# Kernel tuning notes

Hardware: AMD Instinct MI355X
Metric: run time of the kernel (lower is better)

## Reference

```python
import jax, jax.numpy as jnp
import numpy as np

B, S, N, E = 8, 32, 512, 8192
RC = DC = 64; SC = 256; EC = 512; P = 12


def setup_inputs() -> dict:
    key = jax.random.key(0)
    ks = jax.random.split(key, 20)
    def rn(k, shape, s=0.05):
        return jax.random.normal(k, shape, jnp.float32) * s
    return {
        "x": jax.random.normal(ks[0], (B, S, N), jnp.float32),
        "edge_index": jax.random.randint(ks[1], (2, E), 0, N),
        "edge_weight": jax.random.uniform(ks[2], (E,), jnp.float32),
        "start_w": rn(ks[3], (RC, 1)), "start_b": rn(ks[4], (RC,)),
        "filt_w": rn(ks[5], (DC, RC, 2)), "filt_b": rn(ks[6], (DC,)),
        "gate_w": rn(ks[7], (DC, RC, 2)), "gate_b": rn(ks[8], (DC,)),
        "gcn_w": rn(ks[9], (DC, DC)), "gcn_b": rn(ks[10], (DC,)),
        "res_w": rn(ks[11], (RC, DC)), "res_b": rn(ks[12], (RC,)),
        "skip_w": rn(ks[13], (SC, DC)), "skip_b": rn(ks[14], (SC,)),
        "end1_w": rn(ks[15], (EC, SC)), "end1_b": rn(ks[16], (EC,)),
        "end2_w": rn(ks[17], (P, EC)), "end2_b": rn(ks[18], (P,)),
    }


def _conv1x1(x, w, b):
    # Conv2d kernel (1,1): pure channel mix. x: [B,C,N,T], w: [O,C]
    return jnp.einsum('bcnt,oc->bont', x, w) + b[None, :, None, None]


def _conv_time2(x, w, b):
    return (jnp.einsum('bcnt,oc->bont', x[..., :-1], w[..., 0])
            + jnp.einsum('bcnt,oc->bont', x[..., 1:], w[..., 1])
            + b[None, :, None, None])


def _gcn_adj(edge_index, edge_weight, n):
    # PyG gcn_norm: add self-loops (weight 1), symmetric D^-1/2 (A+I) D^-1/2,
    # aggregation at edge_index[1] (target). Returns dense A_hat[tgt, src].
    ar = jnp.arange(n)
    row = jnp.concatenate([edge_index[0], ar])
    col = jnp.concatenate([edge_index[1], ar])
    w = jnp.concatenate([edge_weight, jnp.ones((n,), edge_weight.dtype)])
    deg = jnp.zeros((n,), w.dtype).at[col].add(w)
    dis = jnp.where(deg > 0, jax.lax.rsqrt(deg), jnp.zeros_like(deg))
    norm = dis[row] * w * dis[col]
    return jnp.zeros((n, n), w.dtype).at[col, row].add(norm)


def reference(x, edge_index, edge_weight, start_w, start_b, filt_w, filt_b,
              gate_w, gate_b, gcn_w, gcn_b, res_w, res_b, skip_w, skip_b,
              end1_w, end1_b, end2_w, end2_b):
    n = x.shape[2]
    A = _gcn_adj(edge_index, edge_weight, n)           # [N,N] sparse->dense (N small)
    h = jnp.transpose(x, (0, 2, 1))[:, None]           # [B,1,N,T]
    h = _conv1x1(h, start_w, start_b)                  # [B,RC,N,T]
    residual = h
    f = _conv_time2(h, filt_w, filt_b)                 # [B,DC,N,T-1]
    g = _conv_time2(h, gate_w, gate_b)
    # GCNConv applied to every (batch, time) slice == batched graph matmul
    fg = jnp.einsum('bcnt,oc->bont', f, gcn_w)         # x @ W^T
    fg = jnp.einsum('mn,bont->bomt', A, fg) + gcn_b[None, :, None, None]
    hg = jnp.tanh(fg) * jax.nn.sigmoid(g)              # gated activation
    skip = _conv1x1(hg, skip_w, skip_b)                # [B,SC,N,T-1]
    h = _conv1x1(hg, res_w, res_b) + residual[..., -hg.shape[3]:]
    out = jax.nn.relu(skip)
    out = jax.nn.relu(_conv1x1(out, end1_w, end1_b))
    out = _conv1x1(out, end2_w, end2_b)                # [B,P,N,T-1]
    # adaptive_avg_pool2d((N,1)) with H already N -> mean over time, squeeze
    return out.mean(axis=3)                            # [B,P,N]
```

## Files before the change

### kernel.cpp

```cpp
#include <hip/hip_runtime.h>

#define B_ 8
#define S_ 32
#define N_ 512
#define E_ 8192
#define T_ 31

typedef __attribute__((ext_vector_type(8))) __bf16 bf16x8;
typedef __attribute__((ext_vector_type(4))) float f32x4;
typedef unsigned short u16;
typedef unsigned int u32;

__device__ __forceinline__ u16 f2b(float f) {
    union { float f; u32 u; } v; v.f = f;
    u32 r = v.u + 0x7FFF + ((v.u >> 16) & 1);
    return (u16)(r >> 16);
}

__device__ __forceinline__ u32 cvtpk(float lo, float hi) {
    u32 r;
    asm("v_cvt_pk_bf16_f32 %0, %1, %2" : "=v"(r) : "v"(lo), "v"(hi));
    return r;
}

__device__ __forceinline__ f32x4 mfma16(bf16x8 a, bf16x8 b, f32x4 c) {
    return __builtin_amdgcn_mfma_f32_16x16x32_bf16(a, b, c, 0, 0, 0);
}

__global__ void deg_k(const int* __restrict__ ei, const float* __restrict__ ew,
                      float* __restrict__ deg) {
    int e = blockIdx.x * 256 + threadIdx.x;
    if (e >= E_ + N_) return;
    int col; float w;
    if (e < E_) { col = ei[E_ + e]; w = ew[e]; }
    else        { col = e - E_;     w = 1.f;  }
    atomicAdd(deg + col, w);
}

__global__ void dis_coef_k(const float* __restrict__ deg, float* __restrict__ dis,
                           const float* __restrict__ start_w, const float* __restrict__ start_b,
                           const float* __restrict__ filt_w, const float* __restrict__ filt_b,
                           const float* __restrict__ gate_w, const float* __restrict__ gate_b,
                           const float* __restrict__ gcn_w, float* __restrict__ coef,
                           const float* __restrict__ end2_b, float* __restrict__ out) {
    if (blockIdx.x >= 3) {
        int i = (blockIdx.x - 3) * 256 + threadIdx.x;
        out[i] = end2_b[(i >> 9) % 12];
        return;
    }
    if (blockIdx.x < 2) {
        int n = blockIdx.x * 256 + threadIdx.x;
        float d = deg[n];
        dis[n] = (d > 0.f) ? rsqrtf(d) : 0.f;
        return;
    }
    __shared__ float W[16384];
    __shared__ float sw[64], sb[64], A0[64], A1[64], C0[64];
    __shared__ float r0[128][2], r1[128][2], r2[128][2];
    __shared__ float u0s[64][4], u1s[64][4], u2s[64][4];
    const int tid = threadIdx.x;
    if (tid < 64) { sw[tid] = start_w[tid]; sb[tid] = start_b[tid]; }
#pragma unroll
    for (int k = 0; k < 32; ++k) W[tid + k * 256] = filt_w[tid + k * 256];
#pragma unroll
    for (int k = 0; k < 32; ++k) W[8192 + tid + k * 256] = gate_w[tid + k * 256];
    __syncthreads();
    {
        const int task = tid >> 1, half = tid & 1;
        const int o = task & 63;
        const float* Wb = W + ((task >= 64) ? 8192 : 0);
        float a0 = 0, a1 = 0, c = 0;
        for (int rr = 0; rr < 32; ++rr) {
            int r = (half * 32 + rr + o) & 63;
            float f0 = Wb[(o * 64 + r) * 2], f1 = Wb[(o * 64 + r) * 2 + 1];
            a0 += f0 * sw[r]; a1 += f1 * sw[r]; c += (f0 + f1) * sb[r];
        }
        r0[task][half] = a0; r1[task][half] = a1; r2[task][half] = c;
    }
    __syncthreads();
    if (tid < 128) {
        const int o = tid & 63;
        float a0 = r0[tid][0] + r0[tid][1];
        float a1 = r1[tid][0] + r1[tid][1];
        float c  = r2[tid][0] + r2[tid][1];
        if (tid < 64) { A0[o] = a0; A1[o] = a1; C0[o] = c + filt_b[o]; }
        else { coef[192 + o] = a0; coef[256 + o] = a1; coef[320 + o] = c + gate_b[o]; }
    }
    __syncthreads();
#pragma unroll
    for (int k = 0; k < 16; ++k) W[tid + k * 256] = gcn_w[tid + k * 256];
    __syncthreads();
    {
        const int o = tid & 63, q = tid >> 6;
        float u0 = 0, u1 = 0, u2 = 0;
        for (int dd = 0; dd < 16; ++dd) {
            int d = q * 16 + ((dd + o) & 15);
            float g = W[o * 64 + d];
            u0 += g * A0[d]; u1 += g * A1[d]; u2 += g * C0[d];
        }
        u0s[o][q] = u0; u1s[o][q] = u1; u2s[o][q] = u2;
    }
    __syncthreads();
    if (tid < 64) {
        const int o = tid;
        coef[o]       = u0s[o][0] + u0s[o][1] + u0s[o][2] + u0s[o][3];
        coef[64 + o]  = u1s[o][0] + u1s[o][1] + u1s[o][2] + u1s[o][3];
        coef[128 + o] = u2s[o][0] + u2s[o][1] + u2s[o][2] + u2s[o][3];
    }
}

__global__ void scat_wconv_k(const int* __restrict__ ei, const float* __restrict__ ew,
                             const float* __restrict__ dis,
                             const float* __restrict__ skip_w, const float* __restrict__ end1_w,
                             const float* __restrict__ end2_w,
                             u16* __restrict__ W1, u16* __restrict__ W2, u16* __restrict__ W3,
                             float* __restrict__ S, float* __restrict__ rs) {
    const int bid = blockIdx.x;
    if (bid < 512) {
        int i = bid * 256 + threadIdx.x;
        {
            int m = i & 7, lane = (i >> 3) & 63, ii = (i >> 9) & 3;
            int kkI = (i >> 11) & 7, pw = (i >> 14) & 1, wid = (i >> 15) & 3;
            int er = wid * 128 + pw * 64 + ii * 16 + (lane & 15);
            int col = kkI * 32 + (lane >> 4) * 8 + m;
            W2[i] = f2b(end1_w[er * 256 + col]);
        }
        if (i < 16384) {
            int m = i & 7, lane = (i >> 3) & 63, ii = (i >> 9) & 3;
            int kkI = (i >> 11) & 1, wid = (i >> 12) & 3;
            int sr = wid * 64 + ii * 16 + (lane & 15);
            int col = kkI * 32 + (lane >> 4) * 8 + m;
            W1[i] = f2b(skip_w[sr * 64 + col]);
        }
        if (i < 8192) {
            int m = i & 7, lane = (i >> 3) & 63, c = (i >> 9) & 1;
            int pw = (i >> 10) & 1, wid = (i >> 11) & 3;
            int p = lane & 15;
            int k = wid * 128 + pw * 64 + c * 32 + (lane >> 4) * 8 + m;
            int e = (k & 0x1E0) | (((k >> 3) & 3) << 2) | (k & 3) | (((k >> 2) & 1) << 4);
            W3[i] = f2b((p < 12) ? end2_w[p * 512 + e] : 0.f);
        }
        return;
    }
    int e = (bid - 512) * 256 + threadIdx.x;
    if (e >= E_ + N_) return;
    int row, col; float w;
    if (e < E_) { row = ei[e]; col = ei[E_ + e]; w = ew[e]; }
    else        { row = col = e - E_;            w = 1.f;  }
    float nv = dis[row] * w * dis[col];
    atomicAdd(S + row * N_ + col, nv);
    atomicAdd(rs + col, nv);
}

__global__ void y_k(const float* __restrict__ x, const float* __restrict__ S,
                    float* __restrict__ Y) {
    __shared__ float xs[4][128];
    const int tid = threadIdx.x;
    const int m = (blockIdx.x & 1) * 256 + tid;
    const int q = blockIdx.x >> 1;
    const int ns = q * 128;
    const int bt0 = blockIdx.y * 4;
#pragma unroll
    for (int i = 0; i < 2; ++i) {
        int idx = tid + i * 256;
        xs[idx >> 7][idx & 127] = x[(bt0 + (idx >> 7)) * 512 + ns + (idx & 127)];
    }
    __syncthreads();
    float a0 = 0, a1 = 0, a2 = 0, a3 = 0;
#pragma unroll 8
    for (int n = 0; n < 128; ++n) {
        float sv = S[(ns + n) * 512 + m];
        a0 += xs[0][n] * sv; a1 += xs[1][n] * sv;
        a2 += xs[2][n] * sv; a3 += xs[3][n] * sv;
    }
    float* Yd = Y + q * 131072;
    Yd[(bt0 + 0) * 512 + m] = a0; Yd[(bt0 + 1) * 512 + m] = a1;
    Yd[(bt0 + 2) * 512 + m] = a2; Yd[(bt0 + 3) * 512 + m] = a3;
}

__launch_bounds__(256, 2)
__global__ void fused_k(const float* __restrict__ x, const float* __restrict__ Y,
                        const float* __restrict__ rs, const float* __restrict__ coef,
                        const float* __restrict__ gcn_b, const float* __restrict__ skip_b,
                        const float* __restrict__ end1_b,
                        const u16* __restrict__ W1, const u16* __restrict__ W2,
                        const u16* __restrict__ W3, float* __restrict__ out) {
    __shared__ __align__(16) u16 HG[64 * 64];
    __shared__ __align__(16) u16 SK[64 * 256];
    __shared__ float xs0[64], xs1[64], ys0[64], ys1[64], rsl[64];
    __shared__ float cf[384], gb[64], bsk[256], be1[512];

    const int tid = threadIdx.x;
    const int wid = tid >> 6;
    const int lane = tid & 63;
    const int lr = lane & 15;
    const int lh = lane >> 4;

    const int bid = blockIdx.x;
    const int ntile = bid & 7;
    const int btix = bid >> 3;
    const int t = btix % 31;
    const int b = btix / 31;
    const int n0 = ntile * 64;
    const int bt = b * 32 + t;

    bf16x8 a1f[2][4];
    {
        const u16* w1b = W1 + wid * 4096 + lane * 8;
#pragma unroll
        for (int kkI = 0; kkI < 2; ++kkI)
#pragma unroll
            for (int i = 0; i < 4; ++i)
                a1f[kkI][i] = *(const bf16x8*)(w1b + kkI * 2048 + i * 512);
    }

    if (tid < 64) {
        const int a0 = bt * 512 + n0 + tid, a1 = (bt + 1) * 512 + n0 + tid;
        xs0[tid] = x[a0];
        xs1[tid] = x[a1];
        ys0[tid] = Y[a0] + Y[131072 + a0] + Y[262144 + a0] + Y[393216 + a0];
        ys1[tid] = Y[a1] + Y[131072 + a1] + Y[262144 + a1] + Y[393216 + a1];
        rsl[tid] = rs[n0 + tid];
        gb[tid]  = gcn_b[tid];
    }
    cf[tid] = coef[tid];
    if (tid < 128) cf[256 + tid] = coef[256 + tid];
    bsk[tid] = skip_b[tid];
    be1[tid] = end1_b[tid];
    be1[tid + 256] = end1_b[tid + 256];
    __syncthreads();

#pragma unroll
    for (int k = 0; k < 8; ++k) {
        const int v = tid + k * 256;
        const int pix = v >> 5;
        const int o0 = (v & 31) << 1;
        float hv[2];
#pragma unroll
        for (int q = 0; q < 2; ++q) {
            const int o = o0 + q;
            const float fgv = cf[o] * ys0[pix] + cf[64 + o] * ys1[pix]
                            + cf[128 + o] * rsl[pix] + gb[o];
            const float ggv = cf[192 + o] * xs0[pix] + cf[256 + o] * xs1[pix] + cf[320 + o];
            const float e2f = __expf(2.f * fgv);
            const float eg  = __expf(ggv);
            hv[q] = __fdividef((e2f - 1.f) * eg, (e2f + 1.f) * (1.f + eg));
        }
        *(u32*)(HG + (pix << 6) + (o0 ^ ((pix & 7) << 3))) = cvtpk(hv[0], hv[1]);
    }
    __syncthreads();

    {
        f32x4 acc[4][4];
#pragma unroll
        for (int i = 0; i < 4; ++i)
#pragma unroll
            for (int j = 0; j < 4; ++j) acc[i][j] = (f32x4){0.f, 0.f, 0.f, 0.f};
#pragma unroll
        for (int kkI = 0; kkI < 2; ++kkI) {
            const int kb = kkI * 32 + lh * 8;
            bf16x8 bv[4];
#pragma unroll
            for (int j = 0; j < 4; ++j) {
                const int pr = j * 16 + lr;
                bv[j] = *(const bf16x8*)(HG + (pr << 6) + (kb ^ ((pr & 7) << 3)));
            }
#pragma unroll
            for (int i = 0; i < 4; ++i)
#pragma unroll
                for (int j = 0; j < 4; ++j)
                    acc[i][j] = mfma16(a1f[kkI][i], bv[j], acc[i][j]);
        }
#pragma unroll
        for (int i = 0; i < 4; ++i) {
#pragma unroll
            for (int j = 0; j < 4; ++j) {
                const int pix = j * 16 + lr;
                const int xw = (pix & 7) << 3;
                const int s = wid * 64 + i * 16 + lh * 4;
                const u32 w0 = cvtpk(fmaxf(acc[i][j][0] + bsk[s + 0], 0.f),
                                     fmaxf(acc[i][j][1] + bsk[s + 1], 0.f));
                const u32 w1 = cvtpk(fmaxf(acc[i][j][2] + bsk[s + 2], 0.f),
                                     fmaxf(acc[i][j][3] + bsk[s + 3], 0.f));
                *(u32*)(SK + (pix << 8) + (s ^ xw)) = w0;
                *(u32*)(SK + (pix << 8) + ((s + 2) ^ xw)) = w1;
            }
        }
    }
    __syncthreads();

    {
        f32x4 acc_out[4];
#pragma unroll
        for (int j = 0; j < 4; ++j) acc_out[j] = (f32x4){0.f, 0.f, 0.f, 0.f};

#pragma unroll
        for (int pass = 0; pass < 2; ++pass) {
            const int ep = wid * 128 + pass * 64;
            const u16* w2b = W2 + (wid * 2 + pass) * 16384 + lane * 8;
            bf16x8 bfr[2];
#pragma unroll
            for (int c = 0; c < 2; ++c)
                bfr[c] = *(const bf16x8*)(W3 + (wid * 2 + pass) * 1024 + c * 512 + lane * 8);
            f32x4 acc[4][4];
#pragma unroll
            for (int i = 0; i < 4; ++i)
#pragma unroll
                for (int j = 0; j < 4; ++j) acc[i][j] = (f32x4){0.f, 0.f, 0.f, 0.f};
            bf16x8 aC[4];
#pragma unroll
            for (int i = 0; i < 4; ++i)
                aC[i] = *(const bf16x8*)(w2b + i * 512);
#pragma unroll
            for (int kkI = 0; kkI < 8; ++kkI) {
                bf16x8 aN[4];
                if (kkI < 7) {
#pragma unroll
                    for (int i = 0; i < 4; ++i)
                        aN[i] = *(const bf16x8*)(w2b + (kkI + 1) * 2048 + i * 512);
                }
                const int kb = kkI * 32 + lh * 8;
                bf16x8 bv[4];
#pragma unroll
                for (int j = 0; j < 4; ++j) {
                    const int pr = j * 16 + lr;
                    bv[j] = *(const bf16x8*)(SK + (pr << 8) + (kb ^ ((pr & 7) << 3)));
                }
#pragma unroll
                for (int i = 0; i < 4; ++i)
#pragma unroll
                    for (int j = 0; j < 4; ++j)
                        acc[i][j] = mfma16(aC[i], bv[j], acc[i][j]);
                if (kkI < 7) {
#pragma unroll
                    for (int i = 0; i < 4; ++i) aC[i] = aN[i];
                }
            }
            u32 pk[4][4][2];
#pragma unroll
            for (int i = 0; i < 4; ++i) {
#pragma unroll
                for (int j = 0; j < 4; ++j) {
                    const int eb = ep + i * 16 + lh * 4;
                    pk[i][j][0] = cvtpk(fmaxf(acc[i][j][0] + be1[eb + 0], 0.f),
                                        fmaxf(acc[i][j][1] + be1[eb + 1], 0.f));
                    pk[i][j][1] = cvtpk(fmaxf(acc[i][j][2] + be1[eb + 2], 0.f),
                                        fmaxf(acc[i][j][3] + be1[eb + 3], 0.f));
                }
            }
#pragma unroll
            for (int j = 0; j < 4; ++j) {
#pragma unroll
                for (int c = 0; c < 2; ++c) {
                    union { u32 w[4]; bf16x8 v; } af;
                    af.w[0] = pk[2 * c][j][0];
                    af.w[1] = pk[2 * c][j][1];
                    af.w[2] = pk[2 * c + 1][j][0];
                    af.w[3] = pk[2 * c + 1][j][1];
                    acc_out[j] = mfma16(af.v, bfr[c], acc_out[j]);
                }
            }
        }
        __syncthreads();

        float* SKf = (float*)SK;
#pragma unroll
        for (int j = 0; j < 4; ++j)
#pragma unroll
            for (int r = 0; r < 4; ++r)
                SKf[wid * 1024 + (j * 16 + lh * 4 + r) * 16 + lr] = acc_out[j][r];
    }
    __syncthreads();

    {
        const f32x4* Sv = (const f32x4*)SK;
        f32x4 sum = Sv[tid] + Sv[256 + tid] + Sv[512 + tid] + Sv[768 + tid];
        const int pix = tid >> 2;
        const int p0 = (tid & 3) << 2;
        if (p0 < 12) {
#pragma unroll
            for (int r = 0; r < 4; ++r)
                atomicAdd(out + (b * 12 + p0 + r) * 512 + n0 + pix, sum[r] * (1.f / 31.f));
        }
    }
}

extern "C" void kernel_launch(void* const* d_in, const int* in_sizes, int n_in,
                              void* d_out, int out_size, void* d_ws, size_t ws_size,
                              hipStream_t stream) {
    const float* x       = (const float*)d_in[0];
    const int*   ei      = (const int*)  d_in[1];
    const float* ew      = (const float*)d_in[2];
    const float* start_w = (const float*)d_in[3];
    const float* start_b = (const float*)d_in[4];
    const float* filt_w  = (const float*)d_in[5];
    const float* filt_b  = (const float*)d_in[6];
    const float* gate_w  = (const float*)d_in[7];
    const float* gate_b  = (const float*)d_in[8];
    const float* gcn_w   = (const float*)d_in[9];
    const float* gcn_b   = (const float*)d_in[10];
    const float* skip_w  = (const float*)d_in[13];
    const float* skip_b  = (const float*)d_in[14];
    const float* end1_w  = (const float*)d_in[15];
    const float* end1_b  = (const float*)d_in[16];
    const float* end2_w  = (const float*)d_in[17];
    const float* end2_b  = (const float*)d_in[18];
    float* out = (float*)d_out;

    char* ws = (char*)d_ws;
    float* S    = (float*)(ws);
    float* deg  = (float*)(ws + 1048576);
    float* rs   = (float*)(ws + 1050624);
    float* dis  = (float*)(ws + 1052672);
    float* coef = (float*)(ws + 1579008);
    u16*   W1   = (u16*)  (ws + 1580544);
    u16*   W2   = (u16*)  (ws + 1613312);
    u16*   W3   = (u16*)  (ws + 1875456);
    float* Y    = (float*)(ws + 1891840);

    hipMemsetAsync(S, 0, 1048576 + 4096, stream);
    hipLaunchKernelGGL(deg_k,      dim3(34),  dim3(256), 0, stream, ei, ew, deg);
    hipLaunchKernelGGL(dis_coef_k, dim3(195), dim3(256), 0, stream, deg, dis,
                       start_w, start_b, filt_w, filt_b, gate_w, gate_b, gcn_w, coef,
                       end2_b, out);
    hipLaunchKernelGGL(scat_wconv_k, dim3(546), dim3(256), 0, stream, ei, ew, dis,
                       skip_w, end1_w, end2_w, W1, W2, W3, S, rs);
    hipLaunchKernelGGL(y_k,    dim3(8, 64), dim3(256), 0, stream, x, S, Y);
    hipLaunchKernelGGL(fused_k, dim3(1984), dim3(256), 0, stream,
                       x, Y, rs, coef, gcn_b, skip_b, end1_b, W1, W2, W3, out);
}
```

Measured before the change: 83.11 us.

## Fuse memset and degree computation into one kernel; fold biases into MFMA accumulators

Replaces the hipMemsetAsync and the separate deg_k/dis launch with one init kernel. That kernel zeroes the scatter buffer, zeroes rs, and computes node degrees with shared-memory atomics in a single block. In fused_k, skip and end1 biases now initialise the MFMA accumulators through vector LDS loads instead of being added in the epilogue. The end1 loop also prefetches the next SK fragments from LDS alongside the weight fragments. The intent is fewer launches and less epilogue ALU work, at the cost of serialising the degree pass in one block and raising register pressure from the extra prefetch buffers.

```diff
diff --git a/kernel.cpp b/kernel.cpp
--- a/kernel.cpp
+++ b/kernel.cpp
@@ -27,31 +27,40 @@
     return __builtin_amdgcn_mfma_f32_16x16x32_bf16(a, b, c, 0, 0, 0);
 }
 
-__global__ void deg_k(const int* __restrict__ ei, const float* __restrict__ ew,
-                      float* __restrict__ deg) {
-    int e = blockIdx.x * 256 + threadIdx.x;
-    if (e >= E_ + N_) return;
-    int col; float w;
-    if (e < E_) { col = ei[E_ + e]; w = ew[e]; }
-    else        { col = e - E_;     w = 1.f;  }
-    atomicAdd(deg + col, w);
-}
-
-__global__ void dis_coef_k(const float* __restrict__ deg, float* __restrict__ dis,
-                           const float* __restrict__ start_w, const float* __restrict__ start_b,
+__global__ void init_deg_k(const int* __restrict__ ei, const float* __restrict__ ew,
+                           float* __restrict__ S, float* __restrict__ dis,
+                           float* __restrict__ rs) {
+    const int tid = threadIdx.x;
+    if (blockIdx.x < 128) {
+        f32x4* Sv = (f32x4*)S;
+        const int base = blockIdx.x * 512 + tid;
+        Sv[base] = (f32x4){0.f, 0.f, 0.f, 0.f};
+        Sv[base + 256] = (f32x4){0.f, 0.f, 0.f, 0.f};
+        return;
+    }
+    __shared__ float dg[512];
+    dg[tid] = 1.f; dg[tid + 256] = 1.f;
+    rs[tid] = 0.f; rs[tid + 256] = 0.f;
+    __syncthreads();
+#pragma unroll
+    for (int k = 0; k < 32; ++k) {
+        const int e = tid + k * 256;
+        atomicAdd(dg + ei[E_ + e], ew[e]);
+    }
+    __syncthreads();
+    float d0 = dg[tid], d1 = dg[tid + 256];
+    dis[tid]       = (d0 > 0.f) ? rsqrtf(d0) : 0.f;
+    dis[tid + 256] = (d1 > 0.f) ? rsqrtf(d1) : 0.f;
+}
+
+__global__ void coef_out_k(const float* __restrict__ start_w, const float* __restrict__ start_b,
                            const float* __restrict__ filt_w, const float* __restrict__ filt_b,
                            const float* __restrict__ gate_w, const float* __restrict__ gate_b,
                            const float* __restrict__ gcn_w, float* __restrict__ coef,
                            const float* __restrict__ end2_b, float* __restrict__ out) {
-    if (blockIdx.x >= 3) {
-        int i = (blockIdx.x - 3) * 256 + threadIdx.x;
+    if (blockIdx.x >= 1) {
+        int i = (blockIdx.x - 1) * 256 + threadIdx.x;
         out[i] = end2_b[(i >> 9) % 12];
-        return;
-    }
-    if (blockIdx.x < 2) {
-        int n = blockIdx.x * 256 + threadIdx.x;
-        float d = deg[n];
-        dis[n] = (d > 0.f) ? rsqrtf(d) : 0.f;
         return;
     }
     __shared__ float W[16384];
@@ -188,7 +197,8 @@
     __shared__ __align__(16) u16 HG[64 * 64];
     __shared__ __align__(16) u16 SK[64 * 256];
     __shared__ float xs0[64], xs1[64], ys0[64], ys1[64], rsl[64];
-    __shared__ float cf[384], gb[64], bsk[256], be1[512];
+    __shared__ float cf[384], gb[64];
+    __shared__ __align__(16) float bsk[256], be1[512];
 
     const int tid = threadIdx.x;
     const int wid = tid >> 6;
@@ -253,9 +263,11 @@
     {
         f32x4 acc[4][4];
 #pragma unroll
-        for (int i = 0; i < 4; ++i)
-#pragma unroll
-            for (int j = 0; j < 4; ++j) acc[i][j] = (f32x4){0.f, 0.f, 0.f, 0.f};
+        for (int i = 0; i < 4; ++i) {
+            const f32x4 binit = *(const f32x4*)&bsk[wid * 64 + i * 16 + lh * 4];
+#pragma unroll
+            for (int j = 0; j < 4; ++j) acc[i][j] = binit;
+        }
 #pragma unroll
         for (int kkI = 0; kkI < 2; ++kkI) {
             const int kb = kkI * 32 + lh * 8;
@@ -278,10 +290,8 @@
                 const int pix = j * 16 + lr;
                 const int xw = (pix & 7) << 3;
                 const int s = wid * 64 + i * 16 + lh * 4;
-                const u32 w0 = cvtpk(fmaxf(acc[i][j][0] + bsk[s + 0], 0.f),
-                                     fmaxf(acc[i][j][1] + bsk[s + 1], 0.f));
-                const u32 w1 = cvtpk(fmaxf(acc[i][j][2] + bsk[s + 2], 0.f),
-                                     fmaxf(acc[i][j][3] + bsk[s + 3], 0.f));
+                const u32 w0 = cvtpk(fmaxf(acc[i][j][0], 0.f), fmaxf(acc[i][j][1], 0.f));
+                const u32 w1 = cvtpk(fmaxf(acc[i][j][2], 0.f), fmaxf(acc[i][j][3], 0.f));
                 *(u32*)(SK + (pix << 8) + (s ^ xw)) = w0;
                 *(u32*)(SK + (pix << 8) + ((s + 2) ^ xw)) = w1;
             }
@@ -304,48 +314,53 @@
                 bfr[c] = *(const bf16x8*)(W3 + (wid * 2 + pass) * 1024 + c * 512 + lane * 8);
             f32x4 acc[4][4];
 #pragma unroll
-            for (int i = 0; i < 4; ++i)
-#pragma unroll
-                for (int j = 0; j < 4; ++j) acc[i][j] = (f32x4){0.f, 0.f, 0.f, 0.f};
-            bf16x8 aC[4];
+            for (int i = 0; i < 4; ++i) {
+                const f32x4 binit = *(const f32x4*)&be1[ep + i * 16 + lh * 4];
+#pragma unroll
+                for (int j = 0; j < 4; ++j) acc[i][j] = binit;
+            }
+            bf16x8 aC[4], bvC[4];
 #pragma unroll
             for (int i = 0; i < 4; ++i)
                 aC[i] = *(const bf16x8*)(w2b + i * 512);
 #pragma unroll
+            for (int j = 0; j < 4; ++j) {
+                const int pr = j * 16 + lr;
+                bvC[j] = *(const bf16x8*)(SK + (pr << 8) + ((lh * 8) ^ ((pr & 7) << 3)));
+            }
+#pragma unroll
             for (int kkI = 0; kkI < 8; ++kkI) {
-                bf16x8 aN[4];
+                bf16x8 aN[4], bvN[4];
                 if (kkI < 7) {
 #pragma unroll
                     for (int i = 0; i < 4; ++i)
                         aN[i] = *(const bf16x8*)(w2b + (kkI + 1) * 2048 + i * 512);
+                    const int kb = (kkI + 1) * 32 + lh * 8;
+#pragma unroll
+                    for (int j = 0; j < 4; ++j) {
+                        const int pr = j * 16 + lr;
+                        bvN[j] = *(const bf16x8*)(SK + (pr << 8) + (kb ^ ((pr & 7) << 3)));
+                    }
                 }
-                const int kb = kkI * 32 + lh * 8;
-                bf16x8 bv[4];
+#pragma unroll
+                for (int i = 0; i < 4; ++i)
+#pragma unroll
+                    for (int j = 0; j < 4; ++j)
+                        acc[i][j] = mfma16(aC[i], bvC[j], acc[i][j]);
+                if (kkI < 7) {
+#pragma unroll
+                    for (int i = 0; i < 4; ++i) aC[i] = aN[i];
+#pragma unroll
+                    for (int j = 0; j < 4; ++j) bvC[j] = bvN[j];
+                }
+            }
+            u32 pk[4][4][2];
+#pragma unroll
+            for (int i = 0; i < 4; ++i) {
 #pragma unroll
                 for (int j = 0; j < 4; ++j) {
-                    const int pr = j * 16 + lr;
-                    bv[j] = *(const bf16x8*)(SK + (pr << 8) + (kb ^ ((pr & 7) << 3)));
-                }
-#pragma unroll
-                for (int i = 0; i < 4; ++i)
-#pragma unroll
-                    for (int j = 0; j < 4; ++j)
-                        acc[i][j] = mfma16(aC[i], bv[j], acc[i][j]);
-                if (kkI < 7) {
-#pragma unroll
-                    for (int i = 0; i < 4; ++i) aC[i] = aN[i];
-                }
-            }
-            u32 pk[4][4][2];
-#pragma unroll
-            for (int i = 0; i < 4; ++i) {
-#pragma unroll
-                for (int j = 0; j < 4; ++j) {
-                    const int eb = ep + i * 16 + lh * 4;
-                    pk[i][j][0] = cvtpk(fmaxf(acc[i][j][0] + be1[eb + 0], 0.f),
-                                        fmaxf(acc[i][j][1] + be1[eb + 1], 0.f));
-                    pk[i][j][1] = cvtpk(fmaxf(acc[i][j][2] + be1[eb + 2], 0.f),
-                                        fmaxf(acc[i][j][3] + be1[eb + 3], 0.f));
+                    pk[i][j][0] = cvtpk(fmaxf(acc[i][j][0], 0.f), fmaxf(acc[i][j][1], 0.f));
+                    pk[i][j][1] = cvtpk(fmaxf(acc[i][j][2], 0.f), fmaxf(acc[i][j][3], 0.f));
                 }
             }
 #pragma unroll
@@ -409,7 +424,6 @@
 
     char* ws = (char*)d_ws;
     float* S    = (float*)(ws);
-    float* deg  = (float*)(ws + 1048576);
     float* rs   = (float*)(ws + 1050624);
     float* dis  = (float*)(ws + 1052672);
     float* coef = (float*)(ws + 1579008);
@@ -418,9 +432,8 @@
     u16*   W3   = (u16*)  (ws + 1875456);
     float* Y    = (float*)(ws + 1891840);
 
-    hipMemsetAsync(S, 0, 1048576 + 4096, stream);
-    hipLaunchKernelGGL(deg_k,      dim3(34),  dim3(256), 0, stream, ei, ew, deg);
-    hipLaunchKernelGGL(dis_coef_k, dim3(195), dim3(256), 0, stream, deg, dis,
+    hipLaunchKernelGGL(init_deg_k, dim3(129), dim3(256), 0, stream, ei, ew, S, dis, rs);
+    hipLaunchKernelGGL(coef_out_k, dim3(193), dim3(256), 0, stream,
                        start_w, start_b, filt_w, filt_b, gate_w, gate_b, gcn_w, coef,
                        end2_b, out);
     hipLaunchKernelGGL(scat_wconv_k, dim3(546), dim3(256), 0, stream, ei, ew, dis,
```

After: 85.74 us. +3.2%, slower.
